# Kernel tuning notes

Hardware: AMD Instinct MI355X
Metric: run time of the kernel (lower is better)

## Reference

```python
import jax, jax.numpy as jnp
import numpy as np

B, S, D, H = 1, 2048, 4096, 32
HD = D // H  # 128


def _rope_params(seq_len, head_dim, base=10000.0):
    inv_freq = 1.0 / (base ** (np.arange(0, head_dim, 2, dtype=np.float64) / head_dim))
    ang = np.outer(np.arange(seq_len, dtype=np.float64), inv_freq)      # [S, HD/2]
    ang = np.concatenate([ang, ang], axis=-1)                            # [S, HD]
    return jnp.asarray(np.cos(ang), jnp.float32), jnp.asarray(np.sin(ang), jnp.float32)


def _apply_rope(x, cos, sin):
    # x: [B, H, S, HD]; cos/sin: [S, HD]
    half = x.shape[-1] // 2
    x1, x2 = x[..., :half], x[..., half:]
    rotated = jnp.concatenate([-x2, x1], axis=-1)
    return x * cos[None, None] + rotated * sin[None, None]


def setup_inputs() -> dict:
    key = jax.random.key(0)
    ks = jax.random.split(key, 6)
    w_scale = 1.0 / np.sqrt(D)
    X = jax.random.normal(ks[0], (B, S, D), jnp.float32)
    Wq = jax.random.normal(ks[1], (D, D), jnp.float32) * w_scale
    Wk = jax.random.normal(ks[2], (D, D), jnp.float32) * w_scale
    Wv = jax.random.normal(ks[3], (D, D), jnp.float32) * w_scale
    Wo = jax.random.normal(ks[4], (D, D), jnp.float32) * w_scale
    bo = jax.random.normal(ks[5], (D,), jnp.float32) * 0.01
    cos, sin = _rope_params(S, HD)
    return {"X": X, "Wq": Wq, "Wk": Wk, "Wv": Wv, "Wo": Wo, "bo": bo, "cos": cos, "sin": sin}


def reference(X, Wq, Wk, Wv, Wo, bo, cos, sin):
    b, s, d = X.shape
    # nn.Linear: y = x @ W.T
    def split_heads(y):
        return y.reshape(b, s, H, HD).transpose(0, 2, 1, 3)  # [B,H,S,HD]
    q = split_heads(X @ Wq.T)
    k = split_heads(X @ Wk.T)
    v = split_heads(X @ Wv.T)
    q = _apply_rope(q, cos, sin)
    k = _apply_rope(k, cos, sin)
    scores = jnp.einsum('bhqd,bhkd->bhqk', q, k) / np.sqrt(HD).astype(np.float32)
    causal = jnp.tril(jnp.ones((s, s), bool))
    scores = jnp.where(causal[None, None], scores, -jnp.inf)
    attn = jax.nn.softmax(scores, axis=-1)
    out = jnp.einsum('bhqk,bhkd->bhqd', attn, v)  # [B,H,S,HD]
    out = out.transpose(0, 2, 1, 3).reshape(b, s, d)
    return out @ Wo.T + bo
```

## Files before the change

kernel.cpp:

```cpp
#include <hip/hip_runtime.h>

typedef unsigned short u16;
typedef __attribute__((ext_vector_type(8))) short s16x8;
typedef __attribute__((ext_vector_type(4))) float f32x4;

__device__ __forceinline__ u16 f2bf(float f) {
  unsigned u = __float_as_uint(f);
  u += 0x7fffu + ((u >> 16) & 1u);
  return (u16)(u >> 16);
}
__device__ __forceinline__ float bf2f(u16 h) {
  return __uint_as_float(((unsigned)h) << 16);
}

typedef __attribute__((address_space(1))) const void gvoid_t;
typedef __attribute__((address_space(3))) void lvoid_t;
__device__ __forceinline__ void gload_lds16(const void* g, void* l) {
  __builtin_amdgcn_global_load_lds((gvoid_t*)g, (lvoid_t*)l, 16, 0, 0);
}

__global__ void cvt_f32_bf16(const float* __restrict__ in, u16* __restrict__ out, int n) {
  int i = (blockIdx.x * 256 + threadIdx.x) * 4;
  if (i >= n) return;
  float4 v = *(const float4*)(in + i);
  ushort4 o;
  o.x = f2bf(v.x); o.y = f2bf(v.y); o.z = f2bf(v.z); o.w = f2bf(v.w);
  *(ushort4*)(out + i) = o;
}

template<typename OutT, bool BIAS>
__global__ __launch_bounds__(256) void gemm_bt(
    const u16* __restrict__ A, const u16* __restrict__ Bm,
    OutT* __restrict__ C, const float* __restrict__ bias,
    int M, int N, int K)
{
  __shared__ u16 As[128 * 64];
  __shared__ u16 Bs[128 * 64];

  const int t = threadIdx.x;
  const int lane = t & 63, wid = t >> 6;
  const int wm = wid >> 1, wn = wid & 1;
  const int lr = lane & 15, lk = lane >> 4;
  const int m0 = blockIdx.y * 128, n0 = blockIdx.x * 128;

  f32x4 acc[4][4] = {};

  for (int k0 = 0; k0 < K; k0 += 64) {
#pragma unroll
    for (int it = 0; it < 4; ++it) {
      int id = it * 256 + t;
      int r = id >> 3, c8 = (id & 7) << 3;
      gload_lds16(A + (size_t)(m0 + r) * K + k0 + c8, &As[id * 8]);
      gload_lds16(Bm + (size_t)(n0 + r) * K + k0 + c8, &Bs[id * 8]);
    }
    __syncthreads();

#pragma unroll
    for (int kk = 0; kk < 2; ++kk) {
      s16x8 af[4], bf[4];
#pragma unroll
      for (int i = 0; i < 4; ++i) {
        af[i] = *(const s16x8*)&As[(wm * 64 + i * 16 + lr) * 64 + kk * 32 + lk * 8];
        bf[i] = *(const s16x8*)&Bs[(wn * 64 + i * 16 + lr) * 64 + kk * 32 + lk * 8];
      }
#pragma unroll
      for (int i = 0; i < 4; ++i)
#pragma unroll
        for (int j = 0; j < 4; ++j)
          acc[i][j] = __builtin_amdgcn_mfma_f32_16x16x32_bf16(af[i], bf[j], acc[i][j], 0, 0, 0);
    }
    __syncthreads();
  }

#pragma unroll
  for (int i = 0; i < 4; ++i) {
    int row_b = m0 + wm * 64 + i * 16 + lk * 4;
#pragma unroll
    for (int j = 0; j < 4; ++j) {
      int col = n0 + wn * 64 + j * 16 + lr;
      float bv = BIAS ? bias[col] : 0.f;
#pragma unroll
      for (int r = 0; r < 4; ++r) {
        float v = acc[i][j][r] + bv;
        size_t off = (size_t)(row_b + r) * N + col;
        if constexpr (sizeof(OutT) == 2) ((u16*)C)[off] = f2bf(v);
        else                             ((float*)C)[off] = v;
      }
    }
  }
}

__global__ void rope_qk(u16* __restrict__ Q, u16* __restrict__ Kt,
                        const float* __restrict__ cosp, const float* __restrict__ sinp) {
  int i = blockIdx.x * 256 + threadIdx.x;
  int d = i & 63;
  int h = (i >> 6) & 31;
  int s = i >> 11;
  float c = cosp[s * 128 + d], sn = sinp[s * 128 + d];
  size_t base = (size_t)s * 4096 + h * 128 + d;
  float q1 = bf2f(Q[base]), q2 = bf2f(Q[base + 64]);
  Q[base]      = f2bf(q1 * c - q2 * sn);
  Q[base + 64] = f2bf(q2 * c + q1 * sn);
  float k1 = bf2f(Kt[base]), k2 = bf2f(Kt[base + 64]);
  Kt[base]      = f2bf(k1 * c - k2 * sn);
  Kt[base + 64] = f2bf(k2 * c + k1 * sn);
}

__global__ __launch_bounds__(512) void flash_attn(
    const u16* __restrict__ Q, const u16* __restrict__ Kg, const u16* __restrict__ Vg,
    u16* __restrict__ Ctx)
{
  const int D = 4096;
  __shared__ u16 Ks[2][64 * 128];
  __shared__ u16 Vt[2][128 * 64];
  __shared__ u16 Ps[8][16 * 64];

  const int t = threadIdx.x, lane = t & 63, wid = t >> 6;
  const int lr = lane & 15, lk = lane >> 4;

  const int wg = blockIdx.x;
  const int xcd = wg & 7, j = wg >> 3;
  const int bx = 15 - (j >> 2);
  const int h = xcd * 4 + (j & 3);
  const int q0 = bx * 128;
  const int qw0 = q0 + wid * 16;

  s16x8 qf[4];
#pragma unroll
  for (int kc = 0; kc < 4; ++kc)
    qf[kc] = *(const s16x8*)(Q + (size_t)(qw0 + lr) * D + h * 128 + kc * 32 + lk * 8);

  f32x4 o[8] = {};
  float m_r[4] = {-1e30f, -1e30f, -1e30f, -1e30f};
  float l_r[4] = {0.f, 0.f, 0.f, 0.f};

  const int ntiles = 2 * bx + 2;
  const float scale2 = 0.12751779f;

  const int ch = t & 15, kv2 = (t >> 4) * 2;

  {
    const u16* src = Vg + (size_t)kv2 * D + h * 128 + ch * 8;
    s16x8 a0 = *(const s16x8*)src;
    s16x8 a1 = *(const s16x8*)(src + D);
#pragma unroll
    for (int it = 0; it < 2; ++it) {
      int id = it * 512 + t;
      int kv = id >> 4, c0 = id & 15;
      gload_lds16(Kg + (size_t)kv * D + h * 128 + ((c0 ^ (kv & 7)) << 3), &Ks[0][id * 8]);
    }
#pragma unroll
    for (int jj = 0; jj < 8; ++jj) {
      int d = ch * 8 + jj;
      int sw = ((ch ^ jj) & 7) << 3;
      unsigned pr = (unsigned)(u16)a0[jj] | ((unsigned)(u16)a1[jj] << 16);
      *(unsigned*)&Vt[0][d * 64 + (kv2 ^ sw)] = pr;
    }
  }

  for (int kt = 0; kt < ntiles; ++kt) {
    const int b = kt & 1;
    const int kv0 = kt * 64;
    __syncthreads();

    s16x8 a0, a1;
    const bool pf = (kt + 1 < ntiles);
    if (pf) {
      const u16* src = Vg + (size_t)(kv0 + 64 + kv2) * D + h * 128 + ch * 8;
      a0 = *(const s16x8*)src;
      a1 = *(const s16x8*)(src + D);
#pragma unroll
      for (int it = 0; it < 2; ++it) {
        int id = it * 512 + t;
        int kv = id >> 4, c0 = id & 15;
        gload_lds16(Kg + (size_t)(kv0 + 64 + kv) * D + h * 128 + ((c0 ^ (kv & 7)) << 3),
                    &Ks[b ^ 1][id * 8]);
      }
    }

    if (kv0 <= qw0 + 15) {
      const bool masked = (kv0 + 63 > qw0);

      f32x4 st[4] = {};
      __builtin_amdgcn_s_setprio(1);
#pragma unroll
      for (int nt = 0; nt < 4; ++nt) {
        int kv = nt * 16 + lr;
        int sw = kv & 7;
#pragma unroll
        for (int kc = 0; kc < 4; ++kc) {
          s16x8 kf = *(const s16x8*)&Ks[b][kv * 128 + (((4 * kc + lk) ^ sw) << 3)];
          st[nt] = __builtin_amdgcn_mfma_f32_16x16x32_bf16(qf[kc], kf, st[nt], 0, 0, 0);
        }
      }
      __builtin_amdgcn_s_setprio(0);

      float pmax_[4];
#pragma unroll
      for (int r = 0; r < 4; ++r) {
        int q_r = qw0 + lk * 4 + r;
        if (masked) {
#pragma unroll
          for (int nt = 0; nt < 4; ++nt) {
            float sv = st[nt][r] * scale2;
            if (kv0 + nt * 16 + lr > q_r) sv = -1e30f;
            st[nt][r] = sv;
          }
        } else {
#pragma unroll
          for (int nt = 0; nt < 4; ++nt) st[nt][r] *= scale2;
        }
        float pm = fmaxf(fmaxf(st[0][r], st[1][r]), fmaxf(st[2][r], st[3][r]));
        pm = fmaxf(pm, __shfl_xor(pm, 1));
        pm = fmaxf(pm, __shfl_xor(pm, 2));
        pm = fmaxf(pm, __shfl_xor(pm, 4));
        pm = fmaxf(pm, __shfl_xor(pm, 8));
        pmax_[r] = pm;
      }
      bool nr = (pmax_[0] > m_r[0] + 8.f) || (pmax_[1] > m_r[1] + 8.f) ||
                (pmax_[2] > m_r[2] + 8.f) || (pmax_[3] > m_r[3] + 8.f);
      if (__any(nr)) {
#pragma unroll
        for (int r = 0; r < 4; ++r) {
          float mn = fmaxf(m_r[r], pmax_[r]);
          float al = __builtin_amdgcn_exp2f(m_r[r] - mn);
          m_r[r] = mn; l_r[r] *= al;
#pragma unroll
          for (int nb = 0; nb < 8; ++nb) o[nb][r] *= al;
        }
      }
#pragma unroll
      for (int r = 0; r < 4; ++r) {
        int ql = lk * 4 + r;
        int swp = ((ql >> 1) & 7) << 3;
        float ps = 0.f;
#pragma unroll
        for (int nt = 0; nt < 4; ++nt) {
          float pv = __builtin_amdgcn_exp2f(st[nt][r] - m_r[r]);
          ps += pv;
          Ps[wid][ql * 64 + ((nt * 16 + lr) ^ swp)] = f2bf(pv);
        }
        ps += __shfl_xor(ps, 1);
        ps += __shfl_xor(ps, 2);
        ps += __shfl_xor(ps, 4);
        ps += __shfl_xor(ps, 8);
        l_r[r] += ps;
      }
      asm volatile("s_waitcnt lgkmcnt(0)" ::: "memory");

      s16x8 pa[2];
#pragma unroll
      for (int ks = 0; ks < 2; ++ks) {
        int col = (ks * 32 + lk * 8) ^ (((lr >> 1) & 7) << 3);
        pa[ks] = *(const s16x8*)&Ps[wid][lr * 64 + col];
      }

      __builtin_amdgcn_s_setprio(1);
#pragma unroll
      for (int ks = 0; ks < 2; ++ks) {
#pragma unroll
        for (int nb = 0; nb < 8; ++nb) {
          int d = nb * 16 + lr;
          int g = (((d >> 3) ^ d) & 7) << 3;
          s16x8 vf = *(const s16x8*)&Vt[b][d * 64 + ((ks * 32 + lk * 8) ^ g)];
          o[nb] = __builtin_amdgcn_mfma_f32_16x16x32_bf16(pa[ks], vf, o[nb], 0, 0, 0);
        }
      }
      __builtin_amdgcn_s_setprio(0);
    }

    if (pf) {
#pragma unroll
      for (int jj = 0; jj < 8; ++jj) {
        int d = ch * 8 + jj;
        int sw = ((ch ^ jj) & 7) << 3;
        unsigned pr = (unsigned)(u16)a0[jj] | ((unsigned)(u16)a1[jj] << 16);
        *(unsigned*)&Vt[b ^ 1][d * 64 + (kv2 ^ sw)] = pr;
      }
    }
  }

#pragma unroll
  for (int r = 0; r < 4; ++r) {
    float inv = 1.f / l_r[r];
    int q_r = qw0 + lk * 4 + r;
#pragma unroll
    for (int nb = 0; nb < 8; ++nb)
      Ctx[(size_t)q_r * D + h * 128 + nb * 16 + lr] = f2bf(o[nb][r] * inv);
  }
}

extern "C" void kernel_launch(void* const* d_in, const int* in_sizes, int n_in,
                              void* d_out, int out_size, void* d_ws, size_t ws_size,
                              hipStream_t stream) {
  const int S = 2048, D = 4096, H = 32;
  const size_t SD = (size_t)S * D, DD = (size_t)D * D;

  const float* X  = (const float*)d_in[0];
  const float* Wq = (const float*)d_in[1];
  const float* Wk = (const float*)d_in[2];
  const float* Wv = (const float*)d_in[3];
  const float* Wo = (const float*)d_in[4];
  const float* bo = (const float*)d_in[5];
  const float* cs = (const float*)d_in[6];
  const float* sn = (const float*)d_in[7];

  u16* WB = (u16*)d_ws;
  u16* Xb = WB + DD;
  u16* Qb = Xb + SD;
  u16* Kb = Qb + SD;
  u16* Vb = Kb + SD;

  dim3 blk(256);
  dim3 gg(D / 128, S / 128);

  cvt_f32_bf16<<<(int)(SD / 1024), blk, 0, stream>>>(X, Xb, (int)SD);
  cvt_f32_bf16<<<(int)(DD / 1024), blk, 0, stream>>>(Wq, WB, (int)DD);
  gemm_bt<u16, false><<<gg, blk, 0, stream>>>(Xb, WB, Qb, nullptr, S, D, D);
  cvt_f32_bf16<<<(int)(DD / 1024), blk, 0, stream>>>(Wk, WB, (int)DD);
  gemm_bt<u16, false><<<gg, blk, 0, stream>>>(Xb, WB, Kb, nullptr, S, D, D);
  cvt_f32_bf16<<<(int)(DD / 1024), blk, 0, stream>>>(Wv, WB, (int)DD);
  gemm_bt<u16, false><<<gg, blk, 0, stream>>>(Xb, WB, Vb, nullptr, S, D, D);

  rope_qk<<<(S * H * 64) / 256, blk, 0, stream>>>(Qb, Kb, cs, sn);

  flash_attn<<<dim3(512), dim3(512), 0, stream>>>(Qb, Kb, Vb, Xb );

  cvt_f32_bf16<<<(int)(DD / 1024), blk, 0, stream>>>(Wo, WB, (int)DD);
  gemm_bt<float, true><<<gg, blk, 0, stream>>>(Xb, WB, (float*)d_out, bo, S, D, D);
}
```

Baseline: 589.8 us.

## Rewrite projection GEMM with triple-buffered LDS pipeline, XOR swizzle and XCD-aware tiling

Replaces the 128x128 single-buffered GEMM with a 512-thread 128x256 tile kernel that prefetches two k-tiles ahead into a three-stage LDS ring, using vmcnt waits instead of full syncthreads. LDS columns are XOR-swizzled to avoid bank conflicts, and workgroups are remapped so that N tiles are grouped per XCD for L2 locality. MFMA sections are raised in priority. This targets exposed global-load latency and LDS conflicts in the four projection GEMMs, at the cost of hardcoded grid geometry (256 blocks) that only fits S=2048, D=4096, plus roughly 144KB of LDS.

```diff
diff --git a/kernel.cpp b/kernel.cpp
--- a/kernel.cpp
+++ b/kernel.cpp
@@ -29,59 +29,94 @@
 }
 
 template<typename OutT, bool BIAS>
-__global__ __launch_bounds__(256) void gemm_bt(
+__global__ __launch_bounds__(512, 2) void gemm_bt2(
     const u16* __restrict__ A, const u16* __restrict__ Bm,
     OutT* __restrict__ C, const float* __restrict__ bias,
     int M, int N, int K)
 {
-  __shared__ u16 As[128 * 64];
-  __shared__ u16 Bs[128 * 64];
+  __shared__ u16 As[3][128 * 64];
+  __shared__ u16 Bs[3][256 * 64];
 
   const int t = threadIdx.x;
   const int lane = t & 63, wid = t >> 6;
-  const int wm = wid >> 1, wn = wid & 1;
+  const int wm = wid >> 2, wn = wid & 3;
   const int lr = lane & 15, lk = lane >> 4;
-  const int m0 = blockIdx.y * 128, n0 = blockIdx.x * 128;
+
+  const int wg = blockIdx.x;
+  const int xcd = wg & 7, j = wg >> 3;
+  const int m0 = (j & 15) * 128;
+  const int n0 = ((xcd << 1) | (j >> 4)) * 256;
+
+  const int nt = K >> 6;
 
   f32x4 acc[4][4] = {};
 
-  for (int k0 = 0; k0 < K; k0 += 64) {
-#pragma unroll
-    for (int it = 0; it < 4; ++it) {
-      int id = it * 256 + t;
-      int r = id >> 3, c8 = (id & 7) << 3;
-      gload_lds16(A + (size_t)(m0 + r) * K + k0 + c8, &As[id * 8]);
-      gload_lds16(Bm + (size_t)(n0 + r) * K + k0 + c8, &Bs[id * 8]);
-    }
-    __syncthreads();
-
-#pragma unroll
-    for (int kk = 0; kk < 2; ++kk) {
+#define STAGE(KT)                                                              \
+  {                                                                            \
+    const int bu_ = ((unsigned)(KT)) % 3u;                                     \
+    const int k0_ = (KT) << 6;                                                 \
+    _Pragma("unroll")                                                          \
+    for (int it = 0; it < 2; ++it) {                                           \
+      int id = it * 512 + t;                                                   \
+      int r = id >> 3, c0 = id & 7;                                            \
+      gload_lds16(A + (size_t)(m0 + r) * K + k0_ + ((c0 ^ (r & 7)) << 3),      \
+                  &As[bu_][id * 8]);                                           \
+    }                                                                          \
+    _Pragma("unroll")                                                          \
+    for (int it = 0; it < 4; ++it) {                                           \
+      int id = it * 512 + t;                                                   \
+      int r = id >> 3, c0 = id & 7;                                            \
+      gload_lds16(Bm + (size_t)(n0 + r) * K + k0_ + ((c0 ^ (r & 7)) << 3),     \
+                  &Bs[bu_][id * 8]);                                           \
+    }                                                                          \
+  }
+
+  STAGE(0);
+  STAGE(1);
+  asm volatile("s_waitcnt vmcnt(6)" ::: "memory");
+  __builtin_amdgcn_s_barrier();
+
+  for (int kt = 0; kt < nt; ++kt) {
+    const int bu = ((unsigned)kt) % 3u;
+    if (kt + 2 < nt) STAGE(kt + 2);
+
+#pragma unroll
+    for (int ks = 0; ks < 2; ++ks) {
       s16x8 af[4], bf[4];
 #pragma unroll
       for (int i = 0; i < 4; ++i) {
-        af[i] = *(const s16x8*)&As[(wm * 64 + i * 16 + lr) * 64 + kk * 32 + lk * 8];
-        bf[i] = *(const s16x8*)&Bs[(wn * 64 + i * 16 + lr) * 64 + kk * 32 + lk * 8];
-      }
+        int ra = wm * 64 + i * 16 + lr;
+        af[i] = *(const s16x8*)&As[bu][ra * 64 + (((ks * 4 + lk) ^ (ra & 7)) << 3)];
+        int rb = wn * 64 + i * 16 + lr;
+        bf[i] = *(const s16x8*)&Bs[bu][rb * 64 + (((ks * 4 + lk) ^ (rb & 7)) << 3)];
+      }
+      asm volatile("s_waitcnt lgkmcnt(0)" ::: "memory");
+      __builtin_amdgcn_sched_barrier(0);
+      __builtin_amdgcn_s_setprio(1);
 #pragma unroll
       for (int i = 0; i < 4; ++i)
 #pragma unroll
-        for (int j = 0; j < 4; ++j)
-          acc[i][j] = __builtin_amdgcn_mfma_f32_16x16x32_bf16(af[i], bf[j], acc[i][j], 0, 0, 0);
-    }
-    __syncthreads();
-  }
+        for (int jn = 0; jn < 4; ++jn)
+          acc[i][jn] = __builtin_amdgcn_mfma_f32_16x16x32_bf16(af[i], bf[jn], acc[i][jn], 0, 0, 0);
+      __builtin_amdgcn_s_setprio(0);
+    }
+
+    if (kt + 2 < nt)       { asm volatile("s_waitcnt vmcnt(6)" ::: "memory"); }
+    else if (kt + 2 == nt) { asm volatile("s_waitcnt vmcnt(0)" ::: "memory"); }
+    if (kt + 1 < nt) __builtin_amdgcn_s_barrier();
+  }
+#undef STAGE
 
 #pragma unroll
   for (int i = 0; i < 4; ++i) {
     int row_b = m0 + wm * 64 + i * 16 + lk * 4;
 #pragma unroll
-    for (int j = 0; j < 4; ++j) {
-      int col = n0 + wn * 64 + j * 16 + lr;
+    for (int jn = 0; jn < 4; ++jn) {
+      int col = n0 + wn * 64 + jn * 16 + lr;
       float bv = BIAS ? bias[col] : 0.f;
 #pragma unroll
       for (int r = 0; r < 4; ++r) {
-        float v = acc[i][j][r] + bv;
+        float v = acc[i][jn][r] + bv;
         size_t off = (size_t)(row_b + r) * N + col;
         if constexpr (sizeof(OutT) == 2) ((u16*)C)[off] = f2bf(v);
         else                             ((float*)C)[off] = v;
@@ -312,20 +347,21 @@
   u16* Vb = Kb + SD;
 
   dim3 blk(256);
-  dim3 gg(D / 128, S / 128);
+  dim3 g2(256);
+  dim3 b2(512);
 
   cvt_f32_bf16<<<(int)(SD / 1024), blk, 0, stream>>>(X, Xb, (int)SD);
   cvt_f32_bf16<<<(int)(DD / 1024), blk, 0, stream>>>(Wq, WB, (int)DD);
-  gemm_bt<u16, false><<<gg, blk, 0, stream>>>(Xb, WB, Qb, nullptr, S, D, D);
+  gemm_bt2<u16, false><<<g2, b2, 0, stream>>>(Xb, WB, Qb, nullptr, S, D, D);
   cvt_f32_bf16<<<(int)(DD / 1024), blk, 0, stream>>>(Wk, WB, (int)DD);
-  gemm_bt<u16, false><<<gg, blk, 0, stream>>>(Xb, WB, Kb, nullptr, S, D, D);
+  gemm_bt2<u16, false><<<g2, b2, 0, stream>>>(Xb, WB, Kb, nullptr, S, D, D);
   cvt_f32_bf16<<<(int)(DD / 1024), blk, 0, stream>>>(Wv, WB, (int)DD);
-  gemm_bt<u16, false><<<gg, blk, 0, stream>>>(Xb, WB, Vb, nullptr, S, D, D);
+  gemm_bt2<u16, false><<<g2, b2, 0, stream>>>(Xb, WB, Vb, nullptr, S, D, D);
 
   rope_qk<<<(S * H * 64) / 256, blk, 0, stream>>>(Qb, Kb, cs, sn);
 
   flash_attn<<<dim3(512), dim3(512), 0, stream>>>(Qb, Kb, Vb, Xb );
 
   cvt_f32_bf16<<<(int)(DD / 1024), blk, 0, stream>>>(Wo, WB, (int)DD);
-  gemm_bt<float, true><<<gg, blk, 0, stream>>>(Xb, WB, (float*)d_out, bo, S, D, D);
-}
+  gemm_bt2<float, true><<<g2, b2, 0, stream>>>(Xb, WB, (float*)d_out, bo, S, D, D);
+}
```

Measured after the change: 581.0 us. Within noise of the previous version (-1.5%).
